# Kernel tuning notes

Hardware: AMD Instinct MI355X
Metric: run time of the kernel (lower is better)

The kernel has to match this reference:

```python
import jax, jax.numpy as jnp
import numpy as np

DIM = 512

def setup_inputs() -> dict:
    key = jax.random.key(0)
    k1, k2 = jax.random.split(key)
    pq = jax.random.normal(k1, (65536, 2 * DIM), dtype=jnp.float32)
    A = jax.random.normal(k2, (DIM, DIM), dtype=jnp.float32)
    return {"pq": pq, "A": A}

def reference(pq, A):
    # up_or_low == 'up': p' = p + (A + A^T) q ; q' = q
    S = A + A.T  # symmetric (dim, dim)
    p = pq[..., :DIM]
    q = pq[..., DIM:]
    # (A+A^T) q for each row: since S is symmetric, q @ S == q @ S^T
    pterm = jnp.einsum('bd,ed->be', q, S)  # matches mv(S, q) per row
    return jnp.concatenate([p + pterm, q], axis=-1)
```

## Files before the change

### kernel.cpp

```cpp
#include <hip/hip_runtime.h>
#include <hip/hip_bf16.h>

#define DIM 512
#define BM 64

typedef __bf16 bf16x8 __attribute__((ext_vector_type(8)));
typedef float f32x16 __attribute__((ext_vector_type(16)));

union B128 { uint4 u; bf16x8 v; };

__device__ __forceinline__ unsigned short f2bf(float f) {
    union { __hip_bfloat16 b; unsigned short u; } c;
    c.b = __float2bfloat16(f);
    return c.u;
}

__global__ void prep_s_kernel(const float* __restrict__ A,
                              unsigned short* __restrict__ Sf) {
    const int c   = blockIdx.x * 256 + threadIdx.x;
    const int l   = c & 63;
    const int ks  = (c >> 6) & 31;
    const int nt2 = c >> 11;
    const int e   = nt2 * 32 + (l & 31);
    const int d0  = ks * 16 + (l >> 5) * 8;
    float4 r0 = *(const float4*)(A + (size_t)e * DIM + d0);
    float4 r1 = *(const float4*)(A + (size_t)e * DIM + d0 + 4);
    float cl[8];
    #pragma unroll
    for (int j = 0; j < 8; ++j) cl[j] = A[(size_t)(d0 + j) * DIM + e];
    ushort4 o0, o1;
    o0.x = f2bf(r0.x + cl[0]); o0.y = f2bf(r0.y + cl[1]);
    o0.z = f2bf(r0.z + cl[2]); o0.w = f2bf(r0.w + cl[3]);
    o1.x = f2bf(r1.x + cl[4]); o1.y = f2bf(r1.y + cl[5]);
    o1.z = f2bf(r1.z + cl[6]); o1.w = f2bf(r1.w + cl[7]);
    *(ushort4*)(Sf + (size_t)c * 8)     = o0;
    *(ushort4*)(Sf + (size_t)c * 8 + 4) = o1;
}

__global__ __launch_bounds__(512, 4) void fused_gemm_kernel(
        const float* __restrict__ pq,
        const unsigned short* __restrict__ Sf,
        float* __restrict__ out) {
    __shared__ __align__(16) unsigned char smem[65536];
    unsigned short* As = (unsigned short*)smem;
    float*          Cs = (float*)smem;

    const int t  = threadIdx.x;
    const int l  = t & 63;
    const int w  = t >> 6;
    const int wm = w >> 2;
    const int wn = w & 3;
    const int lane31 = l & 31;
    const int half   = l >> 5;
    const int m0 = blockIdx.x * BM;

    #pragma unroll 4
    for (int p = 0; p < 16; ++p) {
        const int u   = p * 512 + t;
        const int row = u >> 7;
        const int col = (u & 127) * 4;
        const size_t goff = (size_t)(m0 + row) * (2 * DIM) + DIM + col;
        float4 qv = *(const float4*)(pq + goff);
        *(float4*)(out + goff) = qv;
        ushort4 qb;
        qb.x = f2bf(qv.x); qb.y = f2bf(qv.y); qb.z = f2bf(qv.z); qb.w = f2bf(qv.w);
        const int mt   = row >> 5;
        const int ks   = col >> 4;
        const int lpos = (row & 31) + ((col >> 3) & 1) * 32;
        const int chunk = (mt * 32 + ks) * 64 + (lpos ^ (ks & 7));
        *(ushort4*)(As + chunk * 8 + (col & 7)) = qb;
    }
    __syncthreads();

    f32x16 acc[4];
    #pragma unroll
    for (int nt = 0; nt < 4; ++nt)
        #pragma unroll
        for (int r = 0; r < 16; ++r) acc[nt][r] = 0.0f;

    #pragma unroll 2
    for (int ks = 0; ks < 32; ++ks) {
        B128 a;
        const int achunk = (wm * 32 + ks) * 64 + (l ^ (ks & 7));
        a.u = *(const uint4*)(As + achunk * 8);
        #pragma unroll
        for (int nt = 0; nt < 4; ++nt) {
            const int nt2 = nt * 4 + wn;
            B128 b;
            b.u = *(const uint4*)(Sf + (size_t)((nt2 * 32 + ks) * 64 + l) * 8);
            acc[nt] = __builtin_amdgcn_mfma_f32_32x32x16_bf16(a.v, b.v, acc[nt], 0, 0, 0);
        }
    }

    #pragma unroll
    for (int h = 0; h < 2; ++h) {
        __syncthreads();
        #pragma unroll
        for (int i = 0; i < 2; ++i) {
            const int nt = 2 * h + i;
            const int colb = 128 * i + 32 * wn + lane31;
            #pragma unroll
            for (int r = 0; r < 16; ++r) {
                const int row = 32 * wm + 4 * half + (r & 3) + 8 * (r >> 2);
                Cs[row * 256 + colb] = acc[nt][r];
            }
        }
        __syncthreads();
        #pragma unroll
        for (int i = 0; i < 8; ++i) {
            const int row = i * 8 + w;
            const int c0  = l * 4;
            float4 v = *(const float4*)(Cs + row * 256 + c0);
            const size_t goff = (size_t)(m0 + row) * (2 * DIM) + 256 * h + c0;
            float4 pv = *(const float4*)(pq + goff);
            v.x += pv.x; v.y += pv.y; v.z += pv.z; v.w += pv.w;
            *(float4*)(out + goff) = v;
        }
    }
}

extern "C" void kernel_launch(void* const* d_in, const int* in_sizes, int n_in,
                              void* d_out, int out_size, void* d_ws, size_t ws_size,
                              hipStream_t stream) {
    const float* pq = (const float*)d_in[0];
    const float* A  = (const float*)d_in[1];
    float* out = (float*)d_out;
    unsigned short* Sf = (unsigned short*)d_ws;

    prep_s_kernel<<<(DIM * DIM / 8) / 256, 256, 0, stream>>>(A, Sf);
    fused_gemm_kernel<<<65536 / BM, 512, 0, stream>>>(pq, Sf, out);
}
```

Baseline: 473.3 us.

## Halve block tile to 32 rows, batch global loads, use nontemporal stores

Shrinks the row tile from 64 to 32 rows with 256-thread blocks, so twice as many blocks run and each uses half the shared memory, which should raise occupancy and improve latency hiding. All q loads are issued before any stores, p values are prefetched ahead of the epilogue barrier, and output writes use nontemporal stores to avoid polluting the cache. In exchange, each block reloads the full S matrix for half as many rows, doubling total S traffic from L2, and register pressure rises from the 16 float4 prefetch buffers.

New measurement: 580.8 us. 22.7% more time.

```diff
diff --git a/kernel.cpp b/kernel.cpp
--- a/kernel.cpp
+++ b/kernel.cpp
@@ -2,17 +2,25 @@
 #include <hip/hip_bf16.h>
 
 #define DIM 512
-#define BM 64
+#define BM 32
 
 typedef __bf16 bf16x8 __attribute__((ext_vector_type(8)));
 typedef float f32x16 __attribute__((ext_vector_type(16)));
+typedef float f32x4  __attribute__((ext_vector_type(4)));
 
 union B128 { uint4 u; bf16x8 v; };
+union PK  { ushort4 h[2]; uint4 u; };
+union F4  { float4 hip; f32x4 cv; };
 
 __device__ __forceinline__ unsigned short f2bf(float f) {
     union { __hip_bfloat16 b; unsigned short u; } c;
     c.b = __float2bfloat16(f);
     return c.u;
+}
+
+__device__ __forceinline__ void nt_store4(const float4& v, float* p) {
+    F4 u; u.hip = v;
+    __builtin_nontemporal_store(u.cv, (f32x4*)p);
 }
 
 __global__ void prep_s_kernel(const float* __restrict__ A,
@@ -37,38 +45,49 @@
     *(ushort4*)(Sf + (size_t)c * 8 + 4) = o1;
 }
 
-__global__ __launch_bounds__(512, 4) void fused_gemm_kernel(
+__global__ __launch_bounds__(256, 4) void fused_gemm_kernel(
         const float* __restrict__ pq,
         const unsigned short* __restrict__ Sf,
         float* __restrict__ out) {
-    __shared__ __align__(16) unsigned char smem[65536];
+    __shared__ __align__(16) unsigned char smem[32768];
     unsigned short* As = (unsigned short*)smem;
     float*          Cs = (float*)smem;
 
-    const int t  = threadIdx.x;
-    const int l  = t & 63;
-    const int w  = t >> 6;
-    const int wm = w >> 2;
-    const int wn = w & 3;
+    const int t = threadIdx.x;
+    const int l = t & 63;
+    const int w = t >> 6;
     const int lane31 = l & 31;
     const int half   = l >> 5;
     const int m0 = blockIdx.x * BM;
 
-    #pragma unroll 4
-    for (int p = 0; p < 16; ++p) {
-        const int u   = p * 512 + t;
-        const int row = u >> 7;
-        const int col = (u & 127) * 4;
-        const size_t goff = (size_t)(m0 + row) * (2 * DIM) + DIM + col;
-        float4 qv = *(const float4*)(pq + goff);
-        *(float4*)(out + goff) = qv;
-        ushort4 qb;
-        qb.x = f2bf(qv.x); qb.y = f2bf(qv.y); qb.z = f2bf(qv.z); qb.w = f2bf(qv.w);
-        const int mt   = row >> 5;
-        const int ks   = col >> 4;
-        const int lpos = (row & 31) + ((col >> 3) & 1) * 32;
-        const int chunk = (mt * 32 + ks) * 64 + (lpos ^ (ks & 7));
-        *(ushort4*)(As + chunk * 8 + (col & 7)) = qb;
+    float4 qv[16];
+    #pragma unroll
+    for (int p = 0; p < 8; ++p) {
+        const int c    = p * 256 + t;
+        const int row  = c >> 6;
+        const int col0 = (c & 63) * 8;
+        const size_t goff = (size_t)(m0 + row) * (2 * DIM) + DIM + col0;
+        qv[2 * p]     = *(const float4*)(pq + goff);
+        qv[2 * p + 1] = *(const float4*)(pq + goff + 4);
+    }
+    #pragma unroll
+    for (int p = 0; p < 8; ++p) {
+        const int c    = p * 256 + t;
+        const int row  = c >> 6;
+        const int w6   = c & 63;
+        const int ks   = w6 >> 1;
+        const int hi   = w6 & 1;
+        const int col0 = w6 * 8;
+        const size_t goff = (size_t)(m0 + row) * (2 * DIM) + DIM + col0;
+        nt_store4(qv[2 * p],     out + goff);
+        nt_store4(qv[2 * p + 1], out + goff + 4);
+        PK pk;
+        pk.h[0].x = f2bf(qv[2 * p].x);     pk.h[0].y = f2bf(qv[2 * p].y);
+        pk.h[0].z = f2bf(qv[2 * p].z);     pk.h[0].w = f2bf(qv[2 * p].w);
+        pk.h[1].x = f2bf(qv[2 * p + 1].x); pk.h[1].y = f2bf(qv[2 * p + 1].y);
+        pk.h[1].z = f2bf(qv[2 * p + 1].z); pk.h[1].w = f2bf(qv[2 * p + 1].w);
+        const int f = (row + 32 * hi) ^ (ks & 7);
+        *(uint4*)(As + (size_t)(ks * 64 + f) * 8) = pk.u;
     }
     __syncthreads();
 
@@ -81,11 +100,10 @@
     #pragma unroll 2
     for (int ks = 0; ks < 32; ++ks) {
         B128 a;
-        const int achunk = (wm * 32 + ks) * 64 + (l ^ (ks & 7));
-        a.u = *(const uint4*)(As + achunk * 8);
+        a.u = *(const uint4*)(As + (size_t)(ks * 64 + (l ^ (ks & 7))) * 8);
         #pragma unroll
         for (int nt = 0; nt < 4; ++nt) {
-            const int nt2 = nt * 4 + wn;
+            const int nt2 = nt * 4 + w;
             B128 b;
             b.u = *(const uint4*)(Sf + (size_t)((nt2 * 32 + ks) * 64 + l) * 8);
             acc[nt] = __builtin_amdgcn_mfma_f32_32x32x16_bf16(a.v, b.v, acc[nt], 0, 0, 0);
@@ -94,27 +112,36 @@
 
     #pragma unroll
     for (int h = 0; h < 2; ++h) {
+        float4 pv[8];
+        #pragma unroll
+        for (int it = 0; it < 8; ++it) {
+            const int u   = it * 256 + t;
+            const int row = u >> 6;
+            const int c0  = (u & 63) * 4;
+            const size_t goff = (size_t)(m0 + row) * (2 * DIM) + 256 * h + c0;
+            pv[it] = *(const float4*)(pq + goff);
+        }
         __syncthreads();
         #pragma unroll
         for (int i = 0; i < 2; ++i) {
             const int nt = 2 * h + i;
-            const int colb = 128 * i + 32 * wn + lane31;
+            const int colb = 128 * i + 32 * w + lane31;
             #pragma unroll
             for (int r = 0; r < 16; ++r) {
-                const int row = 32 * wm + 4 * half + (r & 3) + 8 * (r >> 2);
+                const int row = 4 * half + (r & 3) + 8 * (r >> 2);
                 Cs[row * 256 + colb] = acc[nt][r];
             }
         }
         __syncthreads();
         #pragma unroll
-        for (int i = 0; i < 8; ++i) {
-            const int row = i * 8 + w;
-            const int c0  = l * 4;
+        for (int it = 0; it < 8; ++it) {
+            const int u   = it * 256 + t;
+            const int row = u >> 6;
+            const int c0  = (u & 63) * 4;
             float4 v = *(const float4*)(Cs + row * 256 + c0);
             const size_t goff = (size_t)(m0 + row) * (2 * DIM) + 256 * h + c0;
-            float4 pv = *(const float4*)(pq + goff);
-            v.x += pv.x; v.y += pv.y; v.z += pv.z; v.w += pv.w;
-            *(float4*)(out + goff) = v;
+            v.x += pv[it].x; v.y += pv[it].y; v.z += pv[it].z; v.w += pv[it].w;
+            nt_store4(v, out + goff);
         }
     }
 }
@@ -128,5 +155,5 @@
     unsigned short* Sf = (unsigned short*)d_ws;
 
     prep_s_kernel<<<(DIM * DIM / 8) / 256, 256, 0, stream>>>(A, Sf);
-    fused_gemm_kernel<<<65536 / BM, 512, 0, stream>>>(pq, Sf, out);
+    fused_gemm_kernel<<<65536 / BM, 256, 0, stream>>>(pq, Sf, out);
 }
```

## Batch q loads up front and use per-wave swizzled LDS epilogue with prefetched p

Applied to the files above, without the earlier changes.

Issues all 16 q float4 loads before any conversion or stores, so more memory requests are in flight at once. The epilogue now has each wave stage its own 32x64 accumulator tile in a private, XOR-swizzled LDS region, which removes one block-wide barrier per half and reduces bank conflicts. The p values are prefetched into registers before the LDS write. Launch bounds drop the occupancy hint from 4 to 2 to leave room for the extra registers, at the risk of less latency hiding across waves.

Result: slower. 485.7 us (+2.6%).

```diff
diff --git a/kernel.cpp b/kernel.cpp
--- a/kernel.cpp
+++ b/kernel.cpp
@@ -37,7 +37,7 @@
     *(ushort4*)(Sf + (size_t)c * 8 + 4) = o1;
 }
 
-__global__ __launch_bounds__(512, 4) void fused_gemm_kernel(
+__global__ __launch_bounds__(512, 2) void fused_gemm_kernel(
         const float* __restrict__ pq,
         const unsigned short* __restrict__ Sf,
         float* __restrict__ out) {
@@ -45,30 +45,39 @@
     unsigned short* As = (unsigned short*)smem;
     float*          Cs = (float*)smem;
 
-    const int t  = threadIdx.x;
-    const int l  = t & 63;
-    const int w  = t >> 6;
+    const int t = threadIdx.x;
+    const int l = t & 63;
+    const int w = t >> 6;
     const int wm = w >> 2;
     const int wn = w & 3;
     const int lane31 = l & 31;
     const int half   = l >> 5;
     const int m0 = blockIdx.x * BM;
 
-    #pragma unroll 4
+    float4 qv[16];
+    #pragma unroll
+    for (int p = 0; p < 16; ++p) {
+        const int u   = p * 512 + t;
+        const int row = u >> 7;
+        const int col = (u & 127) * 4;
+        qv[p] = *(const float4*)(pq + (size_t)(m0 + row) * (2 * DIM) + DIM + col);
+    }
+    __builtin_amdgcn_sched_barrier(0);
+    #pragma unroll
     for (int p = 0; p < 16; ++p) {
         const int u   = p * 512 + t;
         const int row = u >> 7;
         const int col = (u & 127) * 4;
         const size_t goff = (size_t)(m0 + row) * (2 * DIM) + DIM + col;
-        float4 qv = *(const float4*)(pq + goff);
-        *(float4*)(out + goff) = qv;
+        *(float4*)(out + goff) = qv[p];
         ushort4 qb;
-        qb.x = f2bf(qv.x); qb.y = f2bf(qv.y); qb.z = f2bf(qv.z); qb.w = f2bf(qv.w);
+        qb.x = f2bf(qv[p].x); qb.y = f2bf(qv[p].y);
+        qb.z = f2bf(qv[p].z); qb.w = f2bf(qv[p].w);
         const int mt   = row >> 5;
         const int ks   = col >> 4;
         const int lpos = (row & 31) + ((col >> 3) & 1) * 32;
         const int chunk = (mt * 32 + ks) * 64 + (lpos ^ (ks & 7));
-        *(ushort4*)(As + chunk * 8 + (col & 7)) = qb;
+        *(ushort4*)(As + (size_t)chunk * 8 + (col & 7)) = qb;
     }
     __syncthreads();
 
@@ -82,7 +91,7 @@
     for (int ks = 0; ks < 32; ++ks) {
         B128 a;
         const int achunk = (wm * 32 + ks) * 64 + (l ^ (ks & 7));
-        a.u = *(const uint4*)(As + achunk * 8);
+        a.u = *(const uint4*)(As + (size_t)achunk * 8);
         #pragma unroll
         for (int nt = 0; nt < 4; ++nt) {
             const int nt2 = nt * 4 + wn;
@@ -92,29 +101,40 @@
         }
     }
 
+    const int wbase = w * 2048;
     #pragma unroll
     for (int h = 0; h < 2; ++h) {
-        __syncthreads();
+        float4 pv[8];
+        #pragma unroll
+        for (int it = 0; it < 8; ++it) {
+            const int lrow = it * 4 + (l >> 4);
+            const int f4   = l & 15;
+            const int grow = m0 + 32 * wm + lrow;
+            const int gcol = 128 * (2 * h + (f4 >> 3)) + 32 * wn + (f4 & 7) * 4;
+            pv[it] = *(const float4*)(pq + (size_t)grow * (2 * DIM) + gcol);
+        }
+        if (h == 0) __syncthreads();
         #pragma unroll
         for (int i = 0; i < 2; ++i) {
             const int nt = 2 * h + i;
-            const int colb = 128 * i + 32 * wn + lane31;
             #pragma unroll
             for (int r = 0; r < 16; ++r) {
-                const int row = 32 * wm + 4 * half + (r & 3) + 8 * (r >> 2);
-                Cs[row * 256 + colb] = acc[nt][r];
+                const int lrow = 4 * half + (r & 3) + 8 * (r >> 2);
+                const int c    = 32 * i + lane31;
+                const int g    = (c >> 2) ^ (lrow & 7);
+                Cs[wbase + lrow * 64 + g * 4 + (c & 3)] = acc[nt][r];
             }
         }
-        __syncthreads();
         #pragma unroll
-        for (int i = 0; i < 8; ++i) {
-            const int row = i * 8 + w;
-            const int c0  = l * 4;
-            float4 v = *(const float4*)(Cs + row * 256 + c0);
-            const size_t goff = (size_t)(m0 + row) * (2 * DIM) + 256 * h + c0;
-            float4 pv = *(const float4*)(pq + goff);
-            v.x += pv.x; v.y += pv.y; v.z += pv.z; v.w += pv.w;
-            *(float4*)(out + goff) = v;
+        for (int it = 0; it < 8; ++it) {
+            const int lrow = it * 4 + (l >> 4);
+            const int f4   = l & 15;
+            const int gr   = f4 ^ (lrow & 7);
+            float4 v = *(const float4*)(Cs + wbase + lrow * 64 + gr * 4);
+            const int grow = m0 + 32 * wm + lrow;
+            const int gcol = 128 * (2 * h + (f4 >> 3)) + 32 * wn + (f4 & 7) * 4;
+            v.x += pv[it].x; v.y += pv[it].y; v.z += pv[it].z; v.w += pv[it].w;
+            *(float4*)(out + (size_t)grow * (2 * DIM) + gcol) = v;
         }
     }
 }
```
